# Performance work log

Measured on AMD Instinct MI355X. Metric: run time of the kernel, lower is better.

## Reference

```python
import jax, jax.numpy as jnp
import numpy as np

NEARZERO = 1e-05
NMUL = 1
UH_LEN = 15  # gamma unit-hydrograph kernel length (days)

PHY_BOUNDS = {
    'ddf_min': [0.0, 20.0], 'ddf_plus': [0.0, 20.0], 'Tbm': [-2.0, 3.0],
    'Kcum': [0.01, 0.2], 'fcmin': [0.0, 0.1], 'fcmin_plus': [0.01, 0.25],
    'Ccum': [0.005, 0.05], 'Tbf': [-5.0, 2.0], 'Kf': [0.0, 5.0],
    'exp_fe': [0.0, 1.0], 'ET_efficiency': [0.0, 3.0], 'coef_runoff': [0.0, 1.0],
    'coef_vadose2phreatic': [1e-05, 0.02], 'coef_vadose': [0.0, 0.1],
    'coef_phreatic': [1e-05, 0.01], 'vadose_max_level': [0.001, 500.0],
}
ROUT_BOUNDS = {'alpha1': [0.3, 20.0], 'beta1': [0.01, 5.0], 'alpha2': [0.5, 13.0], 'beta2': [0.15, 1.5]}


def change_param_range(p, b):
    return b[0] + p * (b[1] - b[0])


def gamma_uh(alpha, beta, L=UH_LEN):
    # Discretized gamma unit hydrograph, normalized. alpha, beta: [G]
    t = jnp.arange(L, dtype=jnp.float32) + 0.5  # [L]
    w = t ** (alpha[:, None] - 1.0) * jnp.exp(-t / beta[:, None])  # [G, L]
    return w / jnp.sum(w, axis=1, keepdims=True)


def uh_conv(q, uh):
    # Causal per-grid convolution. q: [T, G], uh: [G, L] -> [T, G]
    T, G = q.shape
    L = uh.shape[1]
    qpad = jnp.concatenate([jnp.zeros((L - 1, G), q.dtype), q], axis=0)
    # shifts[l] = q delayed by l steps
    shifts = jnp.stack([qpad[L - 1 - l:L - 1 - l + T] for l in range(L)], axis=0)  # [L, T, G]
    return jnp.einsum('ltg,gl->tg', shifts, uh)


def setup_inputs() -> dict:
    key = jax.random.key(0)
    k1, k2, k3, k4 = jax.random.split(key, 4)
    T, G = 1460, 5000
    prcp = jax.random.uniform(k1, (T, G), jnp.float32) * 20.0   # mm/day, >= 0
    tmean = jax.random.normal(k2, (T, G), jnp.float32) * 10.0   # deg C, crosses 0
    pet = jax.random.uniform(k3, (T, G), jnp.float32) * 5.0     # mm/day
    x_phy = jnp.stack([prcp, tmean, pet], axis=-1)              # [T, G, 3]
    parameters = jax.random.normal(k4, (T, G, 20), jnp.float32)
    return {'x_phy': x_phy, 'parameters': parameters}


def hmets_forward(x_phy, parameters):
    names = list(PHY_BOUNDS.keys())
    nphy = len(names)
    T, G, _ = x_phy.shape
    # unpack_parameters
    phy = jax.nn.sigmoid(parameters[:, :, :nphy * NMUL]).reshape(T, G, nphy, NMUL)
    rout = jax.nn.sigmoid(parameters[-1, :, nphy * NMUL:])  # [G, 4]
    # descale: dynamic_params is empty -> all params static from last step, [G, NMUL]
    pd = {n: change_param_range(phy[-1, :, i, :], PHY_BOUNDS[n]) for i, n in enumerate(names)}
    rd = {n: change_param_range(rout[:, i], ROUT_BOUNDS[n]) for i, n in enumerate(ROUT_BOUNDS)}
    Vmax = pd['vadose_max_level']

    full = lambda: jnp.full((G, NMUL), NEARZERO, jnp.float32)
    init = (full(), full(), full(), 0.5 * Vmax, full())  # SNOW, WATER_IN_SNOWPACK, CUMSNOWMELT, VADOSE, PHREATIC

    def step(carry, inp):
        S, W, C, V, P = carry
        Pp, Tt, PETt = inp
        Pp = Pp[:, None]; Tt = Tt[:, None]; PETt = PETt[:, None]  # [G, 1] broadcast to nmul
        rain = Pp * (Tt >= 0.0).astype(Pp.dtype)
        snow = Pp * (Tt < 0.0).astype(Pp.dtype)
        # overnight refreezing of liquid water in snowpack
        pot_fr = pd['Kf'] * jnp.maximum(pd['Tbf'] - Tt, NEARZERO) ** pd['exp_fe']
        fr = jnp.minimum(pot_fr, W)
        W = W - fr
        S = S + fr
        # degree-day snowmelt with cumulative-melt-dependent ddf
        ddf = jnp.minimum(pd['ddf_min'] + pd['ddf_plus'], pd['ddf_min'] * (1.0 + pd['Kcum'] * C))
        melt = jnp.minimum(jnp.maximum(ddf * (Tt - pd['Tbm']), 0.0), S + snow)
        S = S + snow - melt
        C = (C + melt) * (S > NEARZERO).astype(S.dtype)
        # snowpack water retention
        wrf = jnp.maximum((pd['fcmin'] + pd['fcmin_plus']) * (1.0 - pd['Ccum'] * C), pd['fcmin'])
        wr = wrf * S
        wtmp = W + melt + rain
        wa = jnp.maximum(wtmp - wr, 0.0)
        W = jnp.where(wa > 0.0, wr, wtmp)
        # evapotranspiration + runoff partitioning
        RET = pd['ET_efficiency'] * PETt
        ratio = V / Vmax
        ht0 = pd['coef_runoff'] * ratio * wa                       # surface runoff
        infil = jnp.maximum(wa - ht0 - RET, 0.0)
        ht1 = pd['coef_runoff'] * ratio * ratio * infil            # delayed runoff
        ht2 = pd['coef_vadose'] * V                                # interflow
        v2p = pd['coef_vadose2phreatic'] * V                       # percolation
        V = V + (infil - ht1) - ht2 - v2p
        over = jnp.maximum(V - Vmax, 0.0)                          # vadose overflow -> delayed runoff
        V = V - over
        ht1 = ht1 + over
        P = P + v2p
        ht3 = pd['coef_phreatic'] * P                              # baseflow
        P = P - ht3
        return (S, W, C, V, P), (ht0, ht1, ht2, ht3)

    forc = (x_phy[:, :, 0], x_phy[:, :, 1], x_phy[:, :, 2])
    _, (ht0, ht1, ht2, ht3) = jax.lax.scan(step, init, forc)  # each [T, G, NMUL]
    # average over nmul components (muwts=None -> uniform mean)
    q_surf = ht0.mean(axis=-1)
    q_del = ht1.mean(axis=-1)
    q_gw = (ht2 + ht3).mean(axis=-1)
    # gamma UH routing
    uh1 = gamma_uh(rd['alpha1'], rd['beta1'])
    uh2 = gamma_uh(rd['alpha2'], rd['beta2'])
    Q = uh_conv(q_surf, uh1) + uh_conv(q_del, uh2) + q_gw  # [T, G]
    return Q


def reference(x_phy, parameters):
    return hmets_forward(x_phy, parameters)
```

## Files before the change

### kernel.cpp

```cpp
#include <hip/hip_runtime.h>

#define T_STEPS 1460
#define G_CELLS 5000
#define NPARAM 20
#define UH_L 15
#define NZ 1e-5f
#define KT 32
#define DCH 10
#define NCH (T_STEPS / DCH)

__device__ __forceinline__ float sigmoidf(float x) {
    return 1.0f / (1.0f + __expf(-x));
}

__device__ __forceinline__ float fast_pow(float x, float y) {
    return __builtin_amdgcn_exp2f(y * __builtin_amdgcn_logf(x));
}

__global__ void uh_kernel(const float* __restrict__ params,
                          float* __restrict__ uh1T, float* __restrict__ uh2T) {
    int g = blockIdx.x * blockDim.x + threadIdx.x;
    if (g >= G_CELLS) return;
    const float* pr = params + ((size_t)(T_STEPS - 1) * G_CELLS + g) * NPARAM;
    float a1 = 0.3f  + sigmoidf(pr[16]) * (20.0f - 0.3f);
    float b1 = 0.01f + sigmoidf(pr[17]) * (5.0f  - 0.01f);
    float a2 = 0.5f  + sigmoidf(pr[18]) * (13.0f - 0.5f);
    float b2 = 0.15f + sigmoidf(pr[19]) * (1.5f  - 0.15f);
    float w1[UH_L], w2[UH_L];
    float s1 = 0.f, s2 = 0.f;
    #pragma unroll
    for (int l = 0; l < UH_L; ++l) {
        float t = (float)l + 0.5f;
        w1[l] = fast_pow(t, a1 - 1.0f) * __expf(-t / b1);
        w2[l] = fast_pow(t, a2 - 1.0f) * __expf(-t / b2);
        s1 += w1[l]; s2 += w2[l];
    }
    float r1 = 1.0f / s1, r2 = 1.0f / s2;
    #pragma unroll
    for (int l = 0; l < UH_L; ++l) {
        uh1T[l * G_CELLS + g] = w1[l] * r1;
        uh2T[l * G_CELLS + g] = w2[l] * r2;
    }
}

__global__ void __launch_bounds__(128, 1) rec_kernel(
        const float* __restrict__ x_phy, const float* __restrict__ params,
        float2* __restrict__ q2, float* __restrict__ qgw) {
    const int lane = threadIdx.x & 63;
    const int wid  = threadIdx.x >> 6;
    const int g    = blockIdx.x * 64 + lane;
    const int gc   = (g < G_CELLS) ? g : (G_CELLS - 1);
    const bool valid = (g < G_CELLS);

    __shared__ float s_wa[2][DCH][64];

    const float* pr = params + ((size_t)(T_STEPS - 1) * G_CELLS + gc) * NPARAM;
    const int STR = G_CELLS * 3;

    const float ddf_min    = sigmoidf(pr[0]) * 20.f;
    const float ddf_plus   = sigmoidf(pr[1]) * 20.f;
    const float Tbm        = -2.f + sigmoidf(pr[2]) * 5.f;
    const float Kcum       = 0.01f + sigmoidf(pr[3]) * 0.19f;
    const float fcmin      = sigmoidf(pr[4]) * 0.1f;
    const float fcmin_plus = 0.01f + sigmoidf(pr[5]) * 0.24f;
    const float Ccum       = 0.005f + sigmoidf(pr[6]) * 0.045f;
    const float Tbf        = -5.f + sigmoidf(pr[7]) * 7.f;
    const float Kf         = sigmoidf(pr[8]) * 5.f;
    const float exp_fe     = sigmoidf(pr[9]);
    const float ddf_sum = ddf_min + ddf_plus;
    const float dmK     = ddf_min * Kcum;
    const float fc_sum  = fcmin + fcmin_plus;
    const float fcC     = fc_sum * Ccum;
    float S = NZ, W = NZ, C = NZ;

    const float ET_eff = sigmoidf(pr[10]) * 3.f;
    const float cr     = sigmoidf(pr[11]);
    const float cvp    = 1e-5f + sigmoidf(pr[12]) * (0.02f - 1e-5f);
    const float cv     = sigmoidf(pr[13]) * 0.1f;
    const float cp     = 1e-5f + sigmoidf(pr[14]) * (0.01f - 1e-5f);
    const float Vmax   = 0.001f + sigmoidf(pr[15]) * (500.f - 0.001f);
    const float invVmax = 1.0f / Vmax;
    float V = 0.5f * Vmax, P = NZ;

    const float* base  = x_phy + (size_t)gc * 3;
    const float* baseE = x_phy + (size_t)gc * 3 + 2;

    float A[DCH][2], B[DCH][2];
    float PA[DCH], PB[DCH];

    auto LOADPT = [&](float (&buf)[DCH][2], int c) {
        const float* pp = base + (size_t)c * DCH * STR;
        #pragma unroll
        for (int j = 0; j < DCH; ++j) { buf[j][0] = pp[0]; buf[j][1] = pp[1]; pp += STR; }
    };
    auto LOADPE = [&](float (&buf)[DCH], int c) {
        const float* pp = baseE + (size_t)c * DCH * STR;
        #pragma unroll
        for (int j = 0; j < DCH; ++j) { buf[j] = *pp; pp += STR; }
    };

    auto SNOW = [&](float (&buf)[DCH][2], int c) {
        #pragma unroll
        for (int j = 0; j < DCH; ++j) {
            float Pp = buf[j][0], Tt = buf[j][1];
            float rain = (Tt >= 0.f) ? Pp : 0.f;
            float snow = Pp - rain;
            float xb   = fmaxf(Tbf - Tt, NZ);
            float pot_fr = Kf * fast_pow(xb, exp_fe);
            float fr   = fminf(pot_fr, W);
            W -= fr; S += fr;
            float ddf  = fminf(ddf_sum, fmaf(dmK, C, ddf_min));
            float Ssn  = S + snow;
            float melt = fminf(fmaxf(ddf * (Tt - Tbm), 0.f), Ssn);
            S = Ssn - melt;
            C = (S > NZ) ? (C + melt) : 0.f;
            float wrf  = fmaxf(fmaf(-fcC, C, fc_sum), fcmin);
            float wr   = wrf * S;
            float wtmp = W + melt + rain;
            float wa   = fmaxf(wtmp - wr, 0.f);
            W = (wa > 0.f) ? wr : wtmp;
            s_wa[c & 1][j][lane] = wa;
        }
    };

    auto VP = [&](float (&pe)[DCH], int c) {
        size_t t0 = (size_t)c * DCH;
        #pragma unroll
        for (int j = 0; j < DCH; ++j) {
            float wa   = s_wa[c & 1][j][lane];
            float RET  = ET_eff * pe[j];
            float ratio = V * invVmax;
            float crr   = cr * ratio;
            float ht0   = crr * wa;
            float infil = fmaxf(wa - ht0 - RET, 0.f);
            float ht1   = crr * ratio * infil;
            float ht2   = cv * V;
            float v2p   = cvp * V;
            V = V + infil - ht1 - ht2 - v2p;
            float over  = fmaxf(V - Vmax, 0.f);
            V -= over; ht1 += over;
            P += v2p;
            float ht3 = cp * P;
            P -= ht3;
            if (valid) {
                q2 [(t0 + j) * G_CELLS + g] = make_float2(ht0, ht1);
                qgw[(t0 + j) * G_CELLS + g] = ht2 + ht3;
            }
        }
    };

    if (wid == 0) {
        LOADPT(A, 0); LOADPT(B, 1);
        SNOW(A, 0);
    } else {
        LOADPE(PA, 0); LOADPE(PB, 1);
    }
    __syncthreads();

    for (int c = 0; c < NCH; ++c) {
        if (wid == 0) {
            if (c + 2 < NCH) LOADPT((c & 1) ? B : A, c + 2);
            if (c + 1 < NCH) SNOW(((c + 1) & 1) ? B : A, c + 1);
        } else {
            VP((c & 1) ? PB : PA, c);
            if (c + 2 < NCH) LOADPE((c & 1) ? PB : PA, c + 2);
        }
        __syncthreads();
    }
}

__global__ void __launch_bounds__(256) fir_kernel(
        const float2* __restrict__ q2, const float* __restrict__ qgw,
        const float* __restrict__ uh1T, const float* __restrict__ uh2T,
        float* __restrict__ out) {
    int g = blockIdx.x * 256 + threadIdx.x;
    if (g >= G_CELLS) return;
    int t0 = blockIdx.y * KT;

    float w1[UH_L], w2[UH_L];
    #pragma unroll
    for (int l = 0; l < UH_L; ++l) {
        w1[l] = uh1T[l * G_CELLS + g];
        w2[l] = uh2T[l * G_CELLS + g];
    }
    float r0[UH_L], r1[UH_L];
    #pragma unroll
    for (int k = 0; k < UH_L - 1; ++k) {
        int tq = t0 - (UH_L - 1) + k;
        if (tq >= 0) {
            float2 v = q2[(size_t)tq * G_CELLS + g];
            r0[k] = v.x; r1[k] = v.y;
        } else { r0[k] = 0.f; r1[k] = 0.f; }
    }
    #pragma unroll
    for (int j = 0; j < KT; ++j) {
        int t = t0 + j;
        if (t < T_STEPS) {
            const int ns = (j + UH_L - 1) % UH_L;
            float2 v = q2[(size_t)t * G_CELLS + g];
            r0[ns] = v.x; r1[ns] = v.y;
            float acc = qgw[(size_t)t * G_CELLS + g];
            #pragma unroll
            for (int l = 0; l < UH_L; ++l) {
                const int idx = (j - l + UH_L - 1) % UH_L;
                acc += r0[idx] * w1[l] + r1[idx] * w2[l];
            }
            out[(size_t)t * G_CELLS + g] = acc;
        }
    }
}

extern "C" void kernel_launch(void* const* d_in, const int* in_sizes, int n_in,
                              void* d_out, int out_size, void* d_ws, size_t ws_size,
                              hipStream_t stream) {
    const float* x_phy  = (const float*)d_in[0];
    const float* params = (const float*)d_in[1];
    float* out = (float*)d_out;

    char* ws = (char*)d_ws;
    float2* q2   = (float2*)ws;
    float*  qgw  = (float*)(ws + (size_t)T_STEPS * G_CELLS * 8);
    float*  uh1T = (float*)(ws + (size_t)T_STEPS * G_CELLS * 12);
    float*  uh2T = uh1T + UH_L * G_CELLS;

    uh_kernel<<<(G_CELLS + 255) / 256, 256, 0, stream>>>(params, uh1T, uh2T);
    rec_kernel<<<(G_CELLS + 63) / 64, 128, 0, stream>>>(x_phy, params, q2, qgw);
    dim3 fgrid((G_CELLS + 255) / 256, (T_STEPS + KT - 1) / KT);
    fir_kernel<<<fgrid, 256, 0, stream>>>(q2, qgw, uh1T, uh2T, out);
}
```

Baseline: 889.8 us.

## Fuse UH weights, recurrence and FIR convolution into one warp-specialized kernel

Merges the unit-hydrograph, recurrence and convolution kernels into a single kernel with three specialized wavefronts: snow, vadose/phreatic, and a FIR consumer. Intermediate runoff components pass through shared memory instead of being written to and re-read from global workspace, which removes the q2/qgw round trip and two launches. The vadose wavefront also folds the first three FIR taps into a partial sum, and prefetch depth grows to triple buffering. The cost is a deeper pipeline, with two extra iterations plus a barrier per chunk, and more registers per thread.

```diff
diff --git a/kernel.cpp b/kernel.cpp
--- a/kernel.cpp
+++ b/kernel.cpp
@@ -5,7 +5,6 @@
 #define NPARAM 20
 #define UH_L 15
 #define NZ 1e-5f
-#define KT 32
 #define DCH 10
 #define NCH (T_STEPS / DCH)
 
@@ -17,76 +16,38 @@
     return __builtin_amdgcn_exp2f(y * __builtin_amdgcn_logf(x));
 }
 
-__global__ void uh_kernel(const float* __restrict__ params,
-                          float* __restrict__ uh1T, float* __restrict__ uh2T) {
-    int g = blockIdx.x * blockDim.x + threadIdx.x;
-    if (g >= G_CELLS) return;
-    const float* pr = params + ((size_t)(T_STEPS - 1) * G_CELLS + g) * NPARAM;
-    float a1 = 0.3f  + sigmoidf(pr[16]) * (20.0f - 0.3f);
-    float b1 = 0.01f + sigmoidf(pr[17]) * (5.0f  - 0.01f);
-    float a2 = 0.5f  + sigmoidf(pr[18]) * (13.0f - 0.5f);
-    float b2 = 0.15f + sigmoidf(pr[19]) * (1.5f  - 0.15f);
-    float w1[UH_L], w2[UH_L];
-    float s1 = 0.f, s2 = 0.f;
-    #pragma unroll
-    for (int l = 0; l < UH_L; ++l) {
-        float t = (float)l + 0.5f;
-        w1[l] = fast_pow(t, a1 - 1.0f) * __expf(-t / b1);
-        w2[l] = fast_pow(t, a2 - 1.0f) * __expf(-t / b2);
-        s1 += w1[l]; s2 += w2[l];
-    }
-    float r1 = 1.0f / s1, r2 = 1.0f / s2;
-    #pragma unroll
-    for (int l = 0; l < UH_L; ++l) {
-        uh1T[l * G_CELLS + g] = w1[l] * r1;
-        uh2T[l * G_CELLS + g] = w2[l] * r2;
-    }
-}
-
-__global__ void __launch_bounds__(128, 1) rec_kernel(
+__global__ void __launch_bounds__(192, 1) fused_kernel(
         const float* __restrict__ x_phy, const float* __restrict__ params,
-        float2* __restrict__ q2, float* __restrict__ qgw) {
+        float* __restrict__ out) {
     const int lane = threadIdx.x & 63;
     const int wid  = threadIdx.x >> 6;
     const int g    = blockIdx.x * 64 + lane;
     const int gc   = (g < G_CELLS) ? g : (G_CELLS - 1);
     const bool valid = (g < G_CELLS);
 
-    __shared__ float s_wa[2][DCH][64];
+    __shared__ float  s_wa[2][DCH][64];
+    __shared__ float2 s_ht[2][DCH][64];
+    __shared__ float  s_p [2][DCH][64];
 
     const float* pr = params + ((size_t)(T_STEPS - 1) * G_CELLS + gc) * NPARAM;
     const int STR = G_CELLS * 3;
 
-    const float ddf_min    = sigmoidf(pr[0]) * 20.f;
-    const float ddf_plus   = sigmoidf(pr[1]) * 20.f;
-    const float Tbm        = -2.f + sigmoidf(pr[2]) * 5.f;
-    const float Kcum       = 0.01f + sigmoidf(pr[3]) * 0.19f;
-    const float fcmin      = sigmoidf(pr[4]) * 0.1f;
-    const float fcmin_plus = 0.01f + sigmoidf(pr[5]) * 0.24f;
-    const float Ccum       = 0.005f + sigmoidf(pr[6]) * 0.045f;
-    const float Tbf        = -5.f + sigmoidf(pr[7]) * 7.f;
-    const float Kf         = sigmoidf(pr[8]) * 5.f;
-    const float exp_fe     = sigmoidf(pr[9]);
-    const float ddf_sum = ddf_min + ddf_plus;
-    const float dmK     = ddf_min * Kcum;
-    const float fc_sum  = fcmin + fcmin_plus;
-    const float fcC     = fc_sum * Ccum;
+    const float* base  = x_phy + (size_t)gc * 3;
+    const float* baseE = base + 2;
+
+    float A[DCH][2], B[DCH][2], Cb[DCH][2];
     float S = NZ, W = NZ, C = NZ;
-
-    const float ET_eff = sigmoidf(pr[10]) * 3.f;
-    const float cr     = sigmoidf(pr[11]);
-    const float cvp    = 1e-5f + sigmoidf(pr[12]) * (0.02f - 1e-5f);
-    const float cv     = sigmoidf(pr[13]) * 0.1f;
-    const float cp     = 1e-5f + sigmoidf(pr[14]) * (0.01f - 1e-5f);
-    const float Vmax   = 0.001f + sigmoidf(pr[15]) * (500.f - 0.001f);
-    const float invVmax = 1.0f / Vmax;
-    float V = 0.5f * Vmax, P = NZ;
-
-    const float* base  = x_phy + (size_t)gc * 3;
-    const float* baseE = x_phy + (size_t)gc * 3 + 2;
-
-    float A[DCH][2], B[DCH][2];
-    float PA[DCH], PB[DCH];
+    float ddf_min = 0.f, Tbm = 0.f, fcmin = 0.f, Tbf = 0.f, Kf = 0.f, exp_fe = 0.f;
+    float ddf_sum = 0.f, dmK = 0.f, fc_sum = 0.f, fcC = 0.f;
+
+    float PA[DCH], PB[DCH], PC[DCH];
+    float ET_eff = 0.f, cr = 0.f, cvp = 0.f, cv = 0.f, cp = 0.f;
+    float Vmax = 0.f, invVmax = 0.f, V = 0.f, P = NZ;
+    float a1p = 0.f, a2p = 0.f, b1p = 0.f, b2p = 0.f;
+
+    float W1t[UH_L], W2t[UH_L];
+
+    float r0[UH_L], r1[UH_L];
 
     auto LOADPT = [&](float (&buf)[DCH][2], int c) {
         const float* pp = base + (size_t)c * DCH * STR;
@@ -98,6 +59,55 @@
         #pragma unroll
         for (int j = 0; j < DCH; ++j) { buf[j] = *pp; pp += STR; }
     };
+
+    if (wid == 0) {
+        ddf_min          = sigmoidf(pr[0]) * 20.f;
+        float ddf_plus   = sigmoidf(pr[1]) * 20.f;
+        Tbm              = -2.f + sigmoidf(pr[2]) * 5.f;
+        float Kcum       = 0.01f + sigmoidf(pr[3]) * 0.19f;
+        fcmin            = sigmoidf(pr[4]) * 0.1f;
+        float fcmin_plus = 0.01f + sigmoidf(pr[5]) * 0.24f;
+        float Ccum       = 0.005f + sigmoidf(pr[6]) * 0.045f;
+        Tbf              = -5.f + sigmoidf(pr[7]) * 7.f;
+        Kf               = sigmoidf(pr[8]) * 5.f;
+        exp_fe           = sigmoidf(pr[9]);
+        ddf_sum = ddf_min + ddf_plus;
+        dmK     = ddf_min * Kcum;
+        fc_sum  = fcmin + fcmin_plus;
+        fcC     = fc_sum * Ccum;
+        LOADPT(A, 0); LOADPT(B, 1); LOADPT(Cb, 2);
+    } else {
+        float a1 = 0.3f  + sigmoidf(pr[16]) * (20.0f - 0.3f);
+        float b1 = 0.01f + sigmoidf(pr[17]) * (5.0f  - 0.01f);
+        float a2 = 0.5f  + sigmoidf(pr[18]) * (13.0f - 0.5f);
+        float b2 = 0.15f + sigmoidf(pr[19]) * (1.5f  - 0.15f);
+        float s1 = 0.f, s2 = 0.f;
+        #pragma unroll
+        for (int l = 0; l < UH_L; ++l) {
+            float t = (float)l + 0.5f;
+            W1t[l] = fast_pow(t, a1 - 1.0f) * __expf(-t / b1);
+            W2t[l] = fast_pow(t, a2 - 1.0f) * __expf(-t / b2);
+            s1 += W1t[l]; s2 += W2t[l];
+        }
+        float rs1 = 1.0f / s1, rs2 = 1.0f / s2;
+        #pragma unroll
+        for (int l = 0; l < UH_L; ++l) { W1t[l] *= rs1; W2t[l] *= rs2; }
+
+        if (wid == 1) {
+            ET_eff = sigmoidf(pr[10]) * 3.f;
+            cr     = sigmoidf(pr[11]);
+            cvp    = 1e-5f + sigmoidf(pr[12]) * (0.02f - 1e-5f);
+            cv     = sigmoidf(pr[13]) * 0.1f;
+            cp     = 1e-5f + sigmoidf(pr[14]) * (0.01f - 1e-5f);
+            Vmax   = 0.001f + sigmoidf(pr[15]) * (500.f - 0.001f);
+            invVmax = 1.0f / Vmax;
+            V = 0.5f * Vmax;
+            LOADPE(PA, 0); LOADPE(PB, 1); LOADPE(PC, 2);
+        } else {
+            #pragma unroll
+            for (int l = 0; l < UH_L; ++l) { r0[l] = 0.f; r1[l] = 0.f; }
+        }
+    }
 
     auto SNOW = [&](float (&buf)[DCH][2], int c) {
         #pragma unroll
@@ -123,8 +133,7 @@
         }
     };
 
-    auto VP = [&](float (&pe)[DCH], int c) {
-        size_t t0 = (size_t)c * DCH;
+    auto VPP = [&](float (&pe)[DCH], int c) {
         #pragma unroll
         for (int j = 0; j < DCH; ++j) {
             float wa   = s_wa[c & 1][j][lane];
@@ -142,72 +151,69 @@
             P += v2p;
             float ht3 = cp * P;
             P -= ht3;
-            if (valid) {
-                q2 [(t0 + j) * G_CELLS + g] = make_float2(ht0, ht1);
-                qgw[(t0 + j) * G_CELLS + g] = ht2 + ht3;
+            float gw = ht2 + ht3;
+            s_ht[c & 1][j][lane] = make_float2(ht0, ht1);
+            float p = gw;
+            p += ht0 * W1t[0] + ht1 * W2t[0];
+            p += a1p * W1t[1] + b1p * W2t[1];
+            p += a2p * W1t[2] + b2p * W2t[2];
+            s_p[c & 1][j][lane] = p;
+            a2p = a1p; a1p = ht0;
+            b2p = b1p; b1p = ht1;
+        }
+    };
+
+    #define FIRR(OFF, cc)                                                      \
+    do {                                                                       \
+        const int c_ = (cc);                                                   \
+        size_t t0 = (size_t)c_ * DCH;                                          \
+        _Pragma("unroll")                                                      \
+        for (int j = 0; j < DCH; ++j) {                                        \
+            float2 h  = s_ht[c_ & 1][j][lane];                                 \
+            float acc = s_p [c_ & 1][j][lane];                                 \
+            r0[((OFF) + j) % UH_L] = h.x;                                      \
+            r1[((OFF) + j) % UH_L] = h.y;                                      \
+            _Pragma("unroll")                                                  \
+            for (int l = 3; l < UH_L; ++l) {                                   \
+                const int idx = ((OFF) + j - l + 2 * UH_L) % UH_L;             \
+                acc += r0[idx] * W1t[l] + r1[idx] * W2t[l];                    \
+            }                                                                  \
+            if (valid) out[(t0 + j) * G_CELLS + g] = acc;                      \
+        }                                                                      \
+    } while (0)
+
+    for (int tau = 0; tau < NCH + 2; ++tau) {
+        if (wid == 0) {
+            if (tau < NCH) {
+                int c = tau;
+                switch (c % 3) {
+                case 0:  SNOW(A, c);  if (c + 3 < NCH) LOADPT(A, c + 3);  break;
+                case 1:  SNOW(B, c);  if (c + 3 < NCH) LOADPT(B, c + 3);  break;
+                default: SNOW(Cb, c); if (c + 3 < NCH) LOADPT(Cb, c + 3); break;
+                }
             }
-        }
-    };
-
-    if (wid == 0) {
-        LOADPT(A, 0); LOADPT(B, 1);
-        SNOW(A, 0);
-    } else {
-        LOADPE(PA, 0); LOADPE(PB, 1);
-    }
-    __syncthreads();
-
-    for (int c = 0; c < NCH; ++c) {
-        if (wid == 0) {
-            if (c + 2 < NCH) LOADPT((c & 1) ? B : A, c + 2);
-            if (c + 1 < NCH) SNOW(((c + 1) & 1) ? B : A, c + 1);
+        } else if (wid == 1) {
+            int c = tau - 1;
+            if (c >= 0 && c < NCH) {
+                switch (c % 3) {
+                case 0:  VPP(PA, c); if (c + 3 < NCH) LOADPE(PA, c + 3); break;
+                case 1:  VPP(PB, c); if (c + 3 < NCH) LOADPE(PB, c + 3); break;
+                default: VPP(PC, c); if (c + 3 < NCH) LOADPE(PC, c + 3); break;
+                }
+            }
         } else {
-            VP((c & 1) ? PB : PA, c);
-            if (c + 2 < NCH) LOADPE((c & 1) ? PB : PA, c + 2);
+            int c = tau - 2;
+            if (c >= 0) {
+                switch (c % 3) {
+                case 0:  FIRR(0,  c); break;
+                case 1:  FIRR(10, c); break;
+                default: FIRR(5,  c); break;
+                }
+            }
         }
         __syncthreads();
     }
-}
-
-__global__ void __launch_bounds__(256) fir_kernel(
-        const float2* __restrict__ q2, const float* __restrict__ qgw,
-        const float* __restrict__ uh1T, const float* __restrict__ uh2T,
-        float* __restrict__ out) {
-    int g = blockIdx.x * 256 + threadIdx.x;
-    if (g >= G_CELLS) return;
-    int t0 = blockIdx.y * KT;
-
-    float w1[UH_L], w2[UH_L];
-    #pragma unroll
-    for (int l = 0; l < UH_L; ++l) {
-        w1[l] = uh1T[l * G_CELLS + g];
-        w2[l] = uh2T[l * G_CELLS + g];
-    }
-    float r0[UH_L], r1[UH_L];
-    #pragma unroll
-    for (int k = 0; k < UH_L - 1; ++k) {
-        int tq = t0 - (UH_L - 1) + k;
-        if (tq >= 0) {
-            float2 v = q2[(size_t)tq * G_CELLS + g];
-            r0[k] = v.x; r1[k] = v.y;
-        } else { r0[k] = 0.f; r1[k] = 0.f; }
-    }
-    #pragma unroll
-    for (int j = 0; j < KT; ++j) {
-        int t = t0 + j;
-        if (t < T_STEPS) {
-            const int ns = (j + UH_L - 1) % UH_L;
-            float2 v = q2[(size_t)t * G_CELLS + g];
-            r0[ns] = v.x; r1[ns] = v.y;
-            float acc = qgw[(size_t)t * G_CELLS + g];
-            #pragma unroll
-            for (int l = 0; l < UH_L; ++l) {
-                const int idx = (j - l + UH_L - 1) % UH_L;
-                acc += r0[idx] * w1[l] + r1[idx] * w2[l];
-            }
-            out[(size_t)t * G_CELLS + g] = acc;
-        }
-    }
+    #undef FIRR
 }
 
 extern "C" void kernel_launch(void* const* d_in, const int* in_sizes, int n_in,
@@ -216,15 +222,7 @@
     const float* x_phy  = (const float*)d_in[0];
     const float* params = (const float*)d_in[1];
     float* out = (float*)d_out;
-
-    char* ws = (char*)d_ws;
-    float2* q2   = (float2*)ws;
-    float*  qgw  = (float*)(ws + (size_t)T_STEPS * G_CELLS * 8);
-    float*  uh1T = (float*)(ws + (size_t)T_STEPS * G_CELLS * 12);
-    float*  uh2T = uh1T + UH_L * G_CELLS;
-
-    uh_kernel<<<(G_CELLS + 255) / 256, 256, 0, stream>>>(params, uh1T, uh2T);
-    rec_kernel<<<(G_CELLS + 63) / 64, 128, 0, stream>>>(x_phy, params, q2, qgw);
-    dim3 fgrid((G_CELLS + 255) / 256, (T_STEPS + KT - 1) / KT);
-    fir_kernel<<<fgrid, 256, 0, stream>>>(q2, qgw, uh1T, uh2T, out);
-}
+    (void)d_ws; (void)ws_size; (void)in_sizes; (void)n_in; (void)out_size;
+
+    fused_kernel<<<(G_CELLS + 63) / 64, 192, 0, stream>>>(x_phy, params, out);
+}
```

New measurement: 874.2 us. No clear change (-1.7%).
